# Kernel tuning notes

Measured on AMD Instinct MI355X. Metric: run time of the kernel, lower is better.

Reference implementation:

```python
import jax, jax.numpy as jnp
import numpy as np

B, T, C, H = 2, 2048, 1024, 16
DH = C // H
EPS = 1e-5


def _rotary(t_len, d_head):
    inv_freq = 1.0 / (10000.0 ** (jnp.arange(0, d_head, 2, dtype=jnp.float32) / d_head))
    t = jnp.arange(t_len, dtype=jnp.float32)
    freqs = t[:, None] * inv_freq[None, :]           # [T, dh/2]
    emb = jnp.concatenate([freqs, freqs], axis=-1)    # [T, dh]
    return jnp.cos(emb), jnp.sin(emb)


def _apply_rope(x, cos, sin):
    # x: [B,H,T,dh]; cos/sin: [T,dh]
    d = x.shape[-1]
    x1, x2 = x[..., : d // 2], x[..., d // 2 :]
    x_rot = jnp.concatenate([-x2, x1], axis=-1)
    return x * cos + x_rot * sin


def _decay_mask(t_len, n_head):
    gammas = 1.0 - 2.0 ** (-5.0 - jnp.arange(n_head, dtype=jnp.float32))  # [H]
    n = jnp.arange(t_len)[:, None]
    m = jnp.arange(t_len)[None, :]
    dist = n - m
    decay = gammas[:, None, None] ** jnp.maximum(dist, 0).astype(jnp.float32)
    return jnp.where(dist[None] >= 0, decay, 0.0)  # [H,T,T]


def setup_inputs() -> dict:
    key = jax.random.key(0)
    ks = jax.random.split(key, 7)
    s = 1.0 / np.sqrt(C)
    return {
        "x": jax.random.normal(ks[0], (B, T, C), dtype=jnp.float32),
        "Wq": jax.random.normal(ks[1], (C, C), dtype=jnp.float32) * s,
        "Wk": jax.random.normal(ks[2], (C, C), dtype=jnp.float32) * s,
        "Wv": jax.random.normal(ks[3], (C, C), dtype=jnp.float32) * s,
        "Wo": jax.random.normal(ks[4], (C, C), dtype=jnp.float32) * s,
        "gn_weight": jnp.ones((C,), dtype=jnp.float32),
        "gn_bias": jnp.zeros((C,), dtype=jnp.float32),
    }


def reference(x, Wq, Wk, Wv, Wo, gn_weight, gn_bias):
    b, t, c = x.shape
    # projections (torch Linear: y = x @ W.T), split heads -> [B,H,T,dh]
    def proj(W):
        return jnp.einsum("btc,oc->bto", x, W).reshape(b, t, H, DH).transpose(0, 2, 1, 3)
    q, k, v = proj(Wq), proj(Wk), proj(Wv)

    cos, sin = _rotary(t, DH)
    q = _apply_rope(q, cos, sin)
    k = _apply_rope(k, cos, sin)

    decay = _decay_mask(t, H)                          # [H,T,T]
    qk = jnp.einsum("bhtd,bhsd->bhts", q, k) * (1.0 / np.sqrt(DH))
    qk = qk * decay[None]
    out = jnp.einsum("bhts,bhsd->bhtd", qk, v)         # [B,H,T,dh]

    # GroupNorm with n_head groups over channels, per token
    out = out.transpose(0, 2, 1, 3)                    # [B,T,H,dh]
    mu = jnp.mean(out, axis=-1, keepdims=True)
    var = jnp.mean((out - mu) ** 2, axis=-1, keepdims=True)
    out = (out - mu) * jax.lax.rsqrt(var + EPS)
    out = out * gn_weight.reshape(H, DH) + gn_bias.reshape(H, DH)

    out = out.reshape(b, t, c)
    return jnp.einsum("btc,oc->bto", out, Wo)
```

## Files before the change

### kernel.cpp

```cpp
#include <hip/hip_runtime.h>
#include <stdint.h>

#define B_ 2
#define T_ 2048
#define C_ 1024
#define H_ 16
#define DH_ 64
#define M_ (B_*T_)

typedef short bhalf8 __attribute__((ext_vector_type(8)));
typedef float floatx4 __attribute__((ext_vector_type(4)));

__device__ __forceinline__ short f2bf(float f) {
  unsigned u = __float_as_uint(f);
  u += 0x7fffu + ((u >> 16) & 1u);
  return (short)(u >> 16);
}
__device__ __forceinline__ float bf2f(short s) {
  return __uint_as_float(((unsigned)(unsigned short)s) << 16);
}

__device__ __forceinline__ void gll16(void* lds_dst, const void* g_src) {
  __builtin_amdgcn_global_load_lds(
      reinterpret_cast<const uint32_t __attribute__((address_space(1)))*>(
          reinterpret_cast<uintptr_t>(g_src)),
      reinterpret_cast<uint32_t __attribute__((address_space(3)))*>(
          reinterpret_cast<uintptr_t>(lds_dst)),
      16, 0, 0);
}

__global__ void cvt_all(
    const float* __restrict__ x,  const float* __restrict__ wq,
    const float* __restrict__ wk, const float* __restrict__ wv,
    const float* __restrict__ wo,
    short* __restrict__ xb, short* __restrict__ wqb, short* __restrict__ wkb,
    short* __restrict__ wvb, short* __restrict__ wob)
{
  int i = blockIdx.x * blockDim.x + threadIdx.x;
  const float* s; short* d; int off;
  if (i < (M_*C_/4)) { s = x; d = xb; off = i; }
  else {
    int j = i - M_*C_/4;
    int w = j >> 18;
    off = j & ((1<<18) - 1);
    s = (w==0) ? wq : (w==1) ? wk : (w==2) ? wv : wo;
    d = (w==0) ? wqb : (w==1) ? wkb : (w==2) ? wvb : wob;
  }
  float4 v = ((const float4*)s)[off];
  short4 o;
  o.x = f2bf(v.x); o.y = f2bf(v.y); o.z = f2bf(v.z); o.w = f2bf(v.w);
  ((short4*)d)[off] = o;
}

__global__ __launch_bounds__(512, 2) void gemm_qkv(
    const short* __restrict__ X,
    const short* __restrict__ Wq, const short* __restrict__ Wk, const short* __restrict__ Wv,
    short* __restrict__ Qb, short* __restrict__ Kb, short* __restrict__ Vt)
{
  __shared__ __align__(16) short As[2][256*64];
  __shared__ __align__(16) short Bs[2][256*64];
  const int tid  = threadIdx.x;
  const int lane = tid & 63;
  const int wid  = tid >> 6;
  const int l15  = lane & 15;
  const int quad = lane >> 4;
  const int wr   = wid >> 2;
  const int wc   = wid & 3;
  const int K    = C_;

  const int bid = blockIdx.x;
  const int wg  = (bid & 7) * 24 + (bid >> 3);
  const int nx  = wg % 12;
  const int m0  = (wg / 12) << 8;

  int kind, nloc;
  const short *Ab, *Bb;
  if (nx < 4)      { kind = 0; nloc = nx << 8;       Ab = X  + (size_t)m0*K;   Bb = Wq + (size_t)nloc*K; }
  else if (nx < 8) { kind = 1; nloc = (nx - 4) << 8; Ab = X  + (size_t)m0*K;   Bb = Wk + (size_t)nloc*K; }
  else             { kind = 2; nloc = (nx - 8) << 8; Ab = Wv + (size_t)nloc*K; Bb = X  + (size_t)m0*K;   }

  const int r_loc = tid >> 3;
  const int g_lin = tid & 7;

  auto stageU = [&](short* lds, const short* g, int q, int k0) {
    int row = (q << 6) + r_loc;
    int gs  = g_lin ^ (row & 7);
    gll16(lds + (q << 12) + (wid << 9), g + (size_t)row * K + k0 + (gs << 3));
  };

  floatx4 acc[8][4] = {};

  stageU(&Bs[0][0], Bb, 0, 0); stageU(&Bs[0][0], Bb, 1, 0);
  stageU(&Bs[0][0], Bb, 2, 0); stageU(&Bs[0][0], Bb, 3, 0);
  stageU(&As[0][0], Ab, 0, 0); stageU(&As[0][0], Ab, 2, 0);
  stageU(&As[0][0], Ab, 1, 0); stageU(&As[0][0], Ab, 3, 0);
  asm volatile("s_waitcnt vmcnt(2)" ::: "memory");
  __builtin_amdgcn_s_barrier();
  __builtin_amdgcn_sched_barrier(0);

  for (int t = 0; t < 16; ++t) {
    const int buf = t & 1, nbuf = buf ^ 1;
    const int kn = (t + 1) << 6;
    const bool pf = (t < 15);
    bhalf8 aF[4], bF[4];

#pragma unroll
    for (int i = 0; i < 4; ++i) {
      int row = (wr << 7) + (i << 4) + l15;
      aF[i] = *(const bhalf8*)&As[buf][(row << 6) + ((quad ^ (row & 7)) << 3)];
    }
#pragma unroll
    for (int n = 0; n < 4; ++n) {
      int row = (wc << 6) + (n << 4) + l15;
      bF[n] = *(const bhalf8*)&Bs[buf][(row << 6) + ((quad ^ (row & 7)) << 3)];
    }
    if (pf) { stageU(&Bs[nbuf][0], Bb, 0, kn); stageU(&Bs[nbuf][0], Bb, 1, kn); }
    __builtin_amdgcn_s_barrier();
    asm volatile("s_waitcnt lgkmcnt(0)" ::: "memory");
    __builtin_amdgcn_sched_barrier(0);
    __builtin_amdgcn_s_setprio(1);
#pragma unroll
    for (int i = 0; i < 4; ++i)
#pragma unroll
      for (int n = 0; n < 4; ++n)
        acc[i][n] = __builtin_amdgcn_mfma_f32_16x16x32_bf16(aF[i], bF[n], acc[i][n], 0, 0, 0);
    __builtin_amdgcn_s_setprio(0);
    asm volatile("s_waitcnt vmcnt(2)" ::: "memory");
    __builtin_amdgcn_s_barrier();
    __builtin_amdgcn_sched_barrier(0);

#pragma unroll
    for (int i = 0; i < 4; ++i) {
      int row = (wr << 7) + ((4 + i) << 4) + l15;
      aF[i] = *(const bhalf8*)&As[buf][(row << 6) + ((quad ^ (row & 7)) << 3)];
    }
    if (pf) { stageU(&Bs[nbuf][0], Bb, 2, kn); stageU(&Bs[nbuf][0], Bb, 3, kn); }
    __builtin_amdgcn_s_barrier();
    asm volatile("s_waitcnt lgkmcnt(0)" ::: "memory");
    __builtin_amdgcn_sched_barrier(0);
    __builtin_amdgcn_s_setprio(1);
#pragma unroll
    for (int i = 0; i < 4; ++i)
#pragma unroll
      for (int n = 0; n < 4; ++n)
        acc[4 + i][n] = __builtin_amdgcn_mfma_f32_16x16x32_bf16(aF[i], bF[n], acc[4 + i][n], 0, 0, 0);
    __builtin_amdgcn_s_setprio(0);
    asm volatile("s_waitcnt vmcnt(4)" ::: "memory");
    __builtin_amdgcn_s_barrier();
    __builtin_amdgcn_sched_barrier(0);

#pragma unroll
    for (int i = 0; i < 4; ++i) {
      int row = (wr << 7) + (i << 4) + l15;
      aF[i] = *(const bhalf8*)&As[buf][(row << 6) + (((4 + quad) ^ (row & 7)) << 3)];
    }
#pragma unroll
    for (int n = 0; n < 4; ++n) {
      int row = (wc << 6) + (n << 4) + l15;
      bF[n] = *(const bhalf8*)&Bs[buf][(row << 6) + (((4 + quad) ^ (row & 7)) << 3)];
    }
    if (pf) { stageU(&As[nbuf][0], Ab, 0, kn); stageU(&As[nbuf][0], Ab, 2, kn); }
    __builtin_amdgcn_s_barrier();
    asm volatile("s_waitcnt lgkmcnt(0)" ::: "memory");
    __builtin_amdgcn_sched_barrier(0);
    __builtin_amdgcn_s_setprio(1);
#pragma unroll
    for (int i = 0; i < 4; ++i)
#pragma unroll
      for (int n = 0; n < 4; ++n)
        acc[i][n] = __builtin_amdgcn_mfma_f32_16x16x32_bf16(aF[i], bF[n], acc[i][n], 0, 0, 0);
    __builtin_amdgcn_s_setprio(0);
    asm volatile("s_waitcnt vmcnt(6)" ::: "memory");
    __builtin_amdgcn_s_barrier();
    __builtin_amdgcn_sched_barrier(0);

#pragma unroll
    for (int i = 0; i < 4; ++i) {
      int row = (wr << 7) + ((4 + i) << 4) + l15;
      aF[i] = *(const bhalf8*)&As[buf][(row << 6) + (((4 + quad) ^ (row & 7)) << 3)];
    }
    if (pf) { stageU(&As[nbuf][0], Ab, 1, kn); stageU(&As[nbuf][0], Ab, 3, kn); }
    __builtin_amdgcn_s_barrier();
    asm volatile("s_waitcnt lgkmcnt(0)" ::: "memory");
    __builtin_amdgcn_sched_barrier(0);
    __builtin_amdgcn_s_setprio(1);
#pragma unroll
    for (int i = 0; i < 4; ++i)
#pragma unroll
      for (int n = 0; n < 4; ++n)
        acc[4 + i][n] = __builtin_amdgcn_mfma_f32_16x16x32_bf16(aF[i], bF[n], acc[4 + i][n], 0, 0, 0);
    __builtin_amdgcn_s_setprio(0);
    asm volatile("s_waitcnt vmcnt(2)" ::: "memory");
    __builtin_amdgcn_s_barrier();
    __builtin_amdgcn_sched_barrier(0);
  }

  if (kind < 2) {
    short* Cb = kind ? Kb : Qb;
    const int hh = (nloc + (wc << 6)) >> 6;
    const float frq0 = exp2f((float)l15        * (-0.4152410118609203f));
    const float frq1 = exp2f((float)(l15 + 16) * (-0.4152410118609203f));
#pragma unroll
    for (int m = 0; m < 8; ++m)
#pragma unroll
      for (int r = 0; r < 4; ++r) {
        int n  = m0 + (wr << 7) + (m << 4) + (quad << 2) + r;
        int bb = n >> 11, tt = n & (T_ - 1);
        size_t base = ((size_t)(bb * H_ + hh) * T_ + tt) * DH_;
        float tf = (float)tt;
        {
          float ang = tf * frq0;
          float sn = __sinf(ang), cs = __cosf(ang);
          float xlo = acc[m][0][r], xhi = acc[m][2][r];
          Cb[base + l15]      = f2bf(xlo * cs - xhi * sn);
          Cb[base + l15 + 32] = f2bf(xhi * cs + xlo * sn);
        }
        {
          float ang = tf * frq1;
          float sn = __sinf(ang), cs = __cosf(ang);
          float xlo = acc[m][1][r], xhi = acc[m][3][r];
          Cb[base + l15 + 16] = f2bf(xlo * cs - xhi * sn);
          Cb[base + l15 + 48] = f2bf(xhi * cs + xlo * sn);
        }
      }
  } else {
#pragma unroll
    for (int m = 0; m < 8; ++m)
#pragma unroll
      for (int r = 0; r < 4; ++r) {
        int o = nloc + (wr << 7) + (m << 4) + (quad << 2) + r;
#pragma unroll
        for (int n = 0; n < 4; ++n) {
          int tk = m0 + (wc << 6) + (n << 4) + l15;
          int bb = tk >> 11, tt = tk & (T_ - 1);
          Vt[(size_t)bb * (C_ * T_) + (size_t)o * T_ + tt] = f2bf(acc[m][n][r]);
        }
      }
  }
}

__global__ __launch_bounds__(256) void gemm_out(
    const short* __restrict__ A, const short* __restrict__ Bm, float* __restrict__ Cf)
{
  __shared__ __align__(16) short As[2][128*32];
  __shared__ __align__(16) short Bs[2][64*32];
  const int tid = threadIdx.x, lane = tid & 63, wv = tid >> 6;
  const int l15 = lane & 15, quad = lane >> 4;
  const int n0 = blockIdx.x << 6;
  const int m0 = blockIdx.y << 7;

  const short* Ab = A  + (size_t)m0 * C_;
  const short* Bb = Bm + (size_t)n0 * C_;

  auto stage = [&](int buf, int k0) {
#pragma unroll
    for (int i = 0; i < 2; ++i) {
      int p = (i<<8) + tid, r = p >> 2, go = (p & 3) ^ ((r >> 1) & 3);
      gll16(&As[buf][((i<<8) + (wv<<6))*8], Ab + (size_t)r*C_ + k0 + (go<<3));
    }
    {
      int p = tid, r = p >> 2, go = (p & 3) ^ ((r >> 1) & 3);
      gll16(&Bs[buf][(wv<<6)*8], Bb + (size_t)r*C_ + k0 + (go<<3));
    }
  };

  floatx4 acc[2][4] = {};
  stage(0, 0);
  int cur = 0;
  for (int it = 0; it < 32; ++it) {
    __syncthreads();
    if (it < 31) stage(cur ^ 1, (it + 1) << 5);
    bhalf8 af[2], bfr[4];
#pragma unroll
    for (int rt = 0; rt < 2; ++rt) {
      int row = (wv<<5) + rt*16 + l15;
      af[rt] = *(const bhalf8*)&As[cur][(row<<5) + ((quad ^ ((row>>1)&3))<<3)];
    }
#pragma unroll
    for (int ct = 0; ct < 4; ++ct) {
      int row = ct*16 + l15;
      bfr[ct] = *(const bhalf8*)&Bs[cur][(row<<5) + ((quad ^ ((row>>1)&3))<<3)];
    }
#pragma unroll
    for (int rt = 0; rt < 2; ++rt)
#pragma unroll
      for (int ct = 0; ct < 4; ++ct)
        acc[rt][ct] = __builtin_amdgcn_mfma_f32_16x16x32_bf16(af[rt], bfr[ct], acc[rt][ct], 0, 0, 0);
    cur ^= 1;
  }

#pragma unroll
  for (int rt = 0; rt < 2; ++rt)
#pragma unroll
    for (int r = 0; r < 4; ++r) {
      int n = m0 + (wv<<5) + rt*16 + quad*4 + r;
#pragma unroll
      for (int ct = 0; ct < 4; ++ct)
        Cf[(size_t)n * C_ + n0 + ct*16 + l15] = acc[rt][ct][r];
    }
}

__global__ __launch_bounds__(256) void transpose_k(
    const short* __restrict__ Kb, short* __restrict__ Kt)
{
  __shared__ short tile[64*66];
  const int idx = blockIdx.x, bh = idx >> 5, tc = idx & 31;
  const int t0 = tc << 6;
  const short* src = Kb + ((size_t)bh*T_ + t0) * DH_;
  int row = threadIdx.x >> 2, c0 = (threadIdx.x & 3) << 4;
  *(int4*)&tile[row*66 + c0]     = *(const int4*)&src[row*64 + c0];
  *(int4*)&tile[row*66 + c0 + 8] = *(const int4*)&src[row*64 + c0 + 8];
  __syncthreads();
  short* dst = Kt + (size_t)bh*DH_*T_;
  int d = threadIdx.x >> 2, k0 = (threadIdx.x & 3) << 4;
  short tmp[16];
#pragma unroll
  for (int i = 0; i < 16; ++i) tmp[i] = tile[(k0 + i)*66 + d];
  *(int4*)&dst[(size_t)d*T_ + t0 + k0]     = *(const int4*)&tmp[0];
  *(int4*)&dst[(size_t)d*T_ + t0 + k0 + 8] = *(const int4*)&tmp[8];
}

__global__ __launch_bounds__(256) void seg_state(
    const short* __restrict__ Kt, const short* __restrict__ Vt,
    short* __restrict__ Pseg)
{
  __shared__ __align__(16) short Ks[2][64*64];
  __shared__ __align__(16) short Vs[2][64*64];
  const int tid = threadIdx.x, lane = tid & 63, wv = tid >> 6;
  const int l15 = lane & 15, quad = lane >> 4;
  const int wrow = wv << 4;
  const int bh = blockIdx.x >> 3, p = blockIdx.x & 7;
  const int h = bh & 15;
  const float log2g = log2f(1.f - exp2f(-5.f - (float)h));
  const float g64 = exp2f(log2g * 64.f);

  float wgt[16];
#pragma unroll
  for (int ks = 0; ks < 2; ++ks)
#pragma unroll
    for (int i = 0; i < 8; ++i)
      wgt[ks*8 + i] = exp2f(log2g * (float)(64 - (ks*32 + (quad<<3) + i)));

  const short* Ktg = Kt + (size_t)bh*DH_*T_;
  const short* Vtg = Vt + (size_t)bh*DH_*T_;

  auto stage = [&](int buf, int jc) {
    const int m0 = ((p<<2) + jc) << 6;
#pragma unroll
    for (int i = 0; i < 2; ++i) {
      int slot = (i<<8) + tid;
      int r = slot >> 3, g = (slot & 7) ^ (r & 7);
      gll16(&Ks[buf][((i<<8) + (wv<<6))*8], Ktg + (size_t)r*T_ + m0 + (g<<3));
      gll16(&Vs[buf][((i<<8) + (wv<<6))*8], Vtg + (size_t)r*T_ + m0 + (g<<3));
    }
  };

  floatx4 acc[4] = {};
  stage(0, 0);
  int cur = 0;
  for (int j = 0; j < 4; ++j) {
    __syncthreads();
    if (j < 3) stage(cur ^ 1, j + 1);
#pragma unroll
    for (int ct = 0; ct < 4; ++ct)
#pragma unroll
      for (int r = 0; r < 4; ++r) acc[ct][r] *= g64;
#pragma unroll
    for (int ks = 0; ks < 2; ++ks) {
      int row = wrow + l15;
      bhalf8 va = *(const bhalf8*)&Vs[cur][(row<<6) + ((((ks<<2)+quad) ^ (row&7))<<3)];
      bhalf8 aw;
#pragma unroll
      for (int i = 0; i < 8; ++i) aw[i] = f2bf(bf2f(va[i]) * wgt[ks*8 + i]);
      bhalf8 bk[4];
#pragma unroll
      for (int ct = 0; ct < 4; ++ct) {
        int kr = ct*16 + l15;
        bk[ct] = *(const bhalf8*)&Ks[cur][(kr<<6) + ((((ks<<2)+quad) ^ (kr&7))<<3)];
      }
#pragma unroll
      for (int ct = 0; ct < 4; ++ct)
        acc[ct] = __builtin_amdgcn_mfma_f32_16x16x32_bf16(aw, bk[ct], acc[ct], 0, 0, 0);
    }
    cur ^= 1;
  }
  size_t base = (size_t)(bh*8 + p) * 2 * 4096;
#pragma unroll
  for (int ct = 0; ct < 4; ++ct)
#pragma unroll
    for (int r = 0; r < 4; ++r) {
      int e = wrow + (quad<<2) + r, d = ct*16 + l15;
      float x = acc[ct][r];
      short hi = f2bf(x);
      short lo = f2bf(x - bf2f(hi));
      Pseg[base + e*64 + d]        = hi;
      Pseg[base + 4096 + e*64 + d] = lo;
    }
}

__global__ __launch_bounds__(256) void retention_chunk(
    const short* __restrict__ Qb, const short* __restrict__ Kb,
    const short* __restrict__ Kt, const short* __restrict__ Vt,
    const short* __restrict__ Pseg,
    const float* __restrict__ gnw, const float* __restrict__ gnb,
    short* __restrict__ Xn)
{
  __shared__ __align__(16) short Vs[64*64];
  __shared__ __align__(16) short Kts[64*64];
  __shared__ __align__(16) short KSs[64*64];
  __shared__ __align__(16) short Sh[64*64];
  __shared__ __align__(16) short Sl[64*64];

  const int tid = threadIdx.x, lane = tid & 63, wv = tid >> 6;
  const int l15 = lane & 15, quad = lane >> 4;
  const int wrow = wv << 4;

  const int idx = blockIdx.x;
  const int bh = idx & 31;
  const int cc = idx >> 5;
  const int c  = ((cc & 7) << 2) | (cc >> 3);
  const int p = c >> 2, j = c & 3;
  const int b = bh >> 4, h = bh & 15;
  const int n0 = c << 6;

  const float log2g = log2f(1.f - exp2f(-5.f - (float)h));
  const float g64 = exp2f(log2g * 64.f);

  const short* Qg  = Qb + ((size_t)bh*T_ + n0 + wrow) * DH_;
  const short* Kg  = Kb + (size_t)bh*T_*DH_;
  const short* Ktg = Kt + (size_t)bh*DH_*T_;
  const short* Vtg = Vt + (size_t)bh*DH_*T_;

  bhalf8 aq[2];
#pragma unroll
  for (int ks = 0; ks < 2; ++ks)
    aq[ks] = *(const bhalf8*)(Qg + (size_t)l15*DH_ + ks*32 + quad*8);

  float rowf[4], colf0[4];
#pragma unroll
  for (int r = 0; r < 4; ++r)
    rowf[r] = exp2f(log2g * (float)(wrow + (quad<<2) + r)) * 0.125f;
#pragma unroll
  for (int ct = 0; ct < 4; ++ct)
    colf0[ct] = exp2f(-log2g * (float)(ct*16 + l15));

  const bool has_state = (c > 0);

  floatx4 st[4] = {};
  if (j > 0) {
    float wgt[16];
#pragma unroll
    for (int ks = 0; ks < 2; ++ks)
#pragma unroll
      for (int i = 0; i < 8; ++i)
        wgt[ks*8 + i] = exp2f(log2g * (float)(64 - (ks*32 + (quad<<3) + i)));
    for (int jp = 0; jp < j; ++jp) {
      if (log2g * (float)((j - 1 - jp) << 6) < -34.f) continue;
      const int m0 = ((p<<2) + jp) << 6;
      __syncthreads();
#pragma unroll
      for (int i = 0; i < 2; ++i) {
        int slot = (i<<8) + tid;
        int r = slot >> 3, g = (slot & 7) ^ (r & 7);
        gll16(&Kts[((i<<8) + (wv<<6))*8], Ktg + (size_t)r*T_ + m0 + (g<<3));
        gll16(&Vs[((i<<8) + (wv<<6))*8],  Vtg + (size_t)r*T_ + m0 + (g<<3));
      }
      __syncthreads();
#pragma unroll
      for (int ct = 0; ct < 4; ++ct)
#pragma unroll
        for (int r = 0; r < 4; ++r) st[ct][r] *= g64;
#pragma unroll
      for (int ks = 0; ks < 2; ++ks) {
        int row = wrow + l15;
        bhalf8 va = *(const bhalf8*)&Vs[(row<<6) + ((((ks<<2)+quad) ^ (row&7))<<3)];
        bhalf8 aw;
#pragma unroll
        for (int i = 0; i < 8; ++i) aw[i] = f2bf(bf2f(va[i]) * wgt[ks*8 + i]);
        bhalf8 bk[4];
#pragma unroll
        for (int ct = 0; ct < 4; ++ct) {
          int kr = ct*16 + l15;
          bk[ct] = *(const bhalf8*)&Kts[(kr<<6) + ((((ks<<2)+quad) ^ (kr&7))<<3)];
        }
#pragma unroll
        for (int ct = 0; ct < 4; ++ct)
          st[ct] = __builtin_amdgcn_mfma_f32_16x16x32_bf16(aw, bk[ct], st[ct], 0, 0, 0);
      }
    }
  }
  for (int pp = 0; pp < p; ++pp) {
    float wexp = log2g * (float)(n0 - ((pp + 1) << 8));
    if (wexp < -34.f) continue;
    float w = exp2f(wexp);
    const short* Pg = Pseg + (size_t)(bh*8 + pp) * 2 * 4096;
#pragma unroll
    for (int ct = 0; ct < 4; ++ct)
#pragma unroll
      for (int r = 0; r < 4; ++r) {
        int e = wrow + (quad<<2) + r, d = ct*16 + l15;
        st[ct][r] += w * (bf2f(Pg[e*64 + d]) + bf2f(Pg[4096 + e*64 + d]));
      }
  }
  if (has_state) {
#pragma unroll
    for (int ct = 0; ct < 4; ++ct)
#pragma unroll
      for (int r = 0; r < 4; ++r) {
        int e = wrow + (quad<<2) + r, d = ct*16 + l15;
        float x = st[ct][r];
        short hi = f2bf(x);
        short lo = f2bf(x - bf2f(hi));
        int addr = (e<<6) + ((((d>>3) ^ (e&7))<<3)) + (d&7);
        Sh[addr] = hi; Sl[addr] = lo;
      }
  }

  __syncthreads();
#pragma unroll
  for (int i = 0; i < 2; ++i) {
    int slot = (i<<8) + tid;
    int r = slot >> 3, g = (slot & 7) ^ (r & 7);
    gll16(&KSs[((i<<8) + (wv<<6))*8], Kg  + (size_t)(n0 + r)*DH_ + (g<<3));
    gll16(&Vs[((i<<8) + (wv<<6))*8],  Vtg + (size_t)r*T_ + n0 + (g<<3));
  }
  __syncthreads();

  floatx4 sacc[4] = {};
#pragma unroll
  for (int ks = 0; ks < 2; ++ks) {
    bhalf8 bk[4];
#pragma unroll
    for (int ct = 0; ct < 4; ++ct) {
      int row = ct*16 + l15;
      bk[ct] = *(const bhalf8*)&KSs[(row<<6) + ((((ks<<2)+quad) ^ (row&7))<<3)];
    }
#pragma unroll
    for (int ct = 0; ct < 4; ++ct)
      sacc[ct] = __builtin_amdgcn_mfma_f32_16x16x32_bf16(aq[ks], bk[ct], sacc[ct], 0, 0, 0);
  }
  __syncthreads();
#pragma unroll
  for (int ct = 0; ct < 4; ++ct) {
    float cf = colf0[ct];
    int colg = (ct<<1) + (l15>>3);
    int m = ct*16 + l15;
#pragma unroll
    for (int r = 0; r < 4; ++r) {
      int row = wrow + (quad<<2) + r;
      float v = (row >= m) ? sacc[ct][r] * (rowf[r] * cf) : 0.f;
      KSs[(row<<6) + ((colg ^ ((row>>1)&7))<<3) + (l15&7)] = f2bf(v);
    }
  }
  floatx4 oacc[4] = {};
#pragma unroll
  for (int ks = 0; ks < 2; ++ks) {
    int row = wrow + l15;
    bhalf8 as_ = *(const bhalf8*)&KSs[(row<<6) + ((((ks<<2)+quad) ^ ((row>>1)&7))<<3)];
    bhalf8 bv[4];
#pragma unroll
    for (int ct = 0; ct < 4; ++ct) {
      int vrow = ct*16 + l15;
      bv[ct] = *(const bhalf8*)&Vs[(vrow<<6) + ((((ks<<2)+quad) ^ (vrow&7))<<3)];
    }
#pragma unroll
    for (int ct = 0; ct < 4; ++ct)
      oacc[ct] = __builtin_amdgcn_mfma_f32_16x16x32_bf16(as_, bv[ct], oacc[ct], 0, 0, 0);
  }

  if (has_state) {
    floatx4 iacc[4] = {};
#pragma unroll
    for (int ks = 0; ks < 2; ++ks) {
      bhalf8 bhf[4], blf[4];
#pragma unroll
      for (int ct = 0; ct < 4; ++ct) {
        int er = ct*16 + l15;
        int ga = ((((ks<<2)+quad) ^ (er&7))<<3);
        bhf[ct] = *(const bhalf8*)&Sh[(er<<6) + ga];
        blf[ct] = *(const bhalf8*)&Sl[(er<<6) + ga];
      }
#pragma unroll
      for (int ct = 0; ct < 4; ++ct) {
        iacc[ct] = __builtin_amdgcn_mfma_f32_16x16x32_bf16(aq[ks], bhf[ct], iacc[ct], 0, 0, 0);
        iacc[ct] = __builtin_amdgcn_mfma_f32_16x16x32_bf16(aq[ks], blf[ct], iacc[ct], 0, 0, 0);
      }
    }
#pragma unroll
    for (int ct = 0; ct < 4; ++ct)
#pragma unroll
      for (int r = 0; r < 4; ++r)
        oacc[ct][r] += rowf[r] * iacc[ct][r];
  }

#pragma unroll
  for (int r = 0; r < 4; ++r) {
    float s1 = oacc[0][r] + oacc[1][r] + oacc[2][r] + oacc[3][r];
    float s2 = oacc[0][r]*oacc[0][r] + oacc[1][r]*oacc[1][r]
             + oacc[2][r]*oacc[2][r] + oacc[3][r]*oacc[3][r];
#pragma unroll
    for (int off = 1; off < 16; off <<= 1) {
      s1 += __shfl_xor(s1, off);
      s2 += __shfl_xor(s2, off);
    }
    float mean = s1 * (1.f/64.f);
    float var  = s2 * (1.f/64.f) - mean*mean;
    float rstd = rsqrtf(var + 1e-5f);
    int t = n0 + wrow + (quad<<2) + r;
    size_t obase = ((size_t)b*T_ + t)*C_ + h*DH_;
#pragma unroll
    for (int ct = 0; ct < 4; ++ct) {
      int d = ct*16 + l15;
      float y = (oacc[ct][r] - mean)*rstd*gnw[h*DH_ + d] + gnb[h*DH_ + d];
      Xn[obase + d] = f2bf(y);
    }
  }
}

extern "C" void kernel_launch(void* const* d_in, const int* in_sizes, int n_in,
                              void* d_out, int out_size, void* d_ws, size_t ws_size,
                              hipStream_t stream) {
  (void)in_sizes; (void)n_in; (void)out_size; (void)ws_size;
  const float* x   = (const float*)d_in[0];
  const float* Wq  = (const float*)d_in[1];
  const float* Wk  = (const float*)d_in[2];
  const float* Wv  = (const float*)d_in[3];
  const float* Wo  = (const float*)d_in[4];
  const float* gnw = (const float*)d_in[5];
  const float* gnb = (const float*)d_in[6];
  float* out = (float*)d_out;

  char* ws = (char*)d_ws;
  short* Xb   = (short*)(ws);
  short* Ktb  = (short*)(ws);
  short* Wqb  = (short*)(ws + (8u<<20));
  short* Pseg = (short*)(ws + (8u<<20));
  short* Wkb  = (short*)(ws + (10u<<20));
  short* Wvb  = (short*)(ws + (12u<<20));
  short* Wob  = (short*)(ws + (14u<<20));
  short* Qb   = (short*)(ws + (16u<<20));
  short* Kb   = (short*)(ws + (24u<<20));
  short* Vtw  = (short*)(ws + (32u<<20));
  short* Xn   = (short*)(ws + (40u<<20));

  cvt_all<<<(M_*C_/4 + 4*(C_*C_/4)) / 256, 256, 0, stream>>>(
      x, Wq, Wk, Wv, Wo, Xb, Wqb, Wkb, Wvb, Wob);

  gemm_qkv<<<dim3(192), 512, 0, stream>>>(Xb, Wqb, Wkb, Wvb, Qb, Kb, Vtw);
  transpose_k<<<1024, 256, 0, stream>>>(Kb, Ktb);
  seg_state<<<256, 256, 0, stream>>>(Ktb, Vtw, Pseg);
  retention_chunk<<<1024, 256, 0, stream>>>(Qb, Kb, Ktb, Vtw, Pseg, gnw, gnb, Xn);
  gemm_out<<<dim3(16, 32), 256, 0, stream>>>(Xn, Wob, out);
}
```

Before: 170.2 us.

## Fuse K transpose into QKV GEMM epilogue and deepen gemm_out K-tile

The K-projection epilogue in gemm_qkv now also writes the rotated K values into a swizzled LDS tile, reusing the GEMM staging buffers, and stores a transposed Kt copy directly. This removes the separate transpose_k kernel launch and its global read/write pass. Kt moves to its own workspace region so it no longer aliases Xb, which is still read by the QKV GEMM. Separately, gemm_out now stages 64-wide K tiles with an 8-way XOR swizzle, halving the number of loop iterations and barriers at the cost of more LDS per block.

Result: faster. 165.5 us (-2.8%).

```diff
diff --git a/kernel.cpp b/kernel.cpp
--- a/kernel.cpp
+++ b/kernel.cpp
@@ -55,10 +55,14 @@
 __global__ __launch_bounds__(512, 2) void gemm_qkv(
     const short* __restrict__ X,
     const short* __restrict__ Wq, const short* __restrict__ Wk, const short* __restrict__ Wv,
-    short* __restrict__ Qb, short* __restrict__ Kb, short* __restrict__ Vt)
+    short* __restrict__ Qb, short* __restrict__ Kb, short* __restrict__ Vt,
+    short* __restrict__ Kt)
 {
-  __shared__ __align__(16) short As[2][256*64];
-  __shared__ __align__(16) short Bs[2][256*64];
+  __shared__ __align__(16) short SM[4*256*64];
+  short (*As)[256*64] = (short (*)[256*64])(SM);
+  short (*Bs)[256*64] = (short (*)[256*64])(SM + 2*256*64);
+  short* Ct = SM;
+
   const int tid  = threadIdx.x;
   const int lane = tid & 63;
   const int wid  = tid >> 6;
@@ -200,29 +204,59 @@
     const int hh = (nloc + (wc << 6)) >> 6;
     const float frq0 = exp2f((float)l15        * (-0.4152410118609203f));
     const float frq1 = exp2f((float)(l15 + 16) * (-0.4152410118609203f));
+    const int swz = (l15 & 7) << 3;
 #pragma unroll
     for (int m = 0; m < 8; ++m)
 #pragma unroll
       for (int r = 0; r < 4; ++r) {
-        int n  = m0 + (wr << 7) + (m << 4) + (quad << 2) + r;
+        int tl = (wr << 7) + (m << 4) + (quad << 2) + r;
+        int n  = m0 + tl;
         int bb = n >> 11, tt = n & (T_ - 1);
         size_t base = ((size_t)(bb * H_ + hh) * T_ + tt) * DH_;
         float tf = (float)tt;
+        float v0, v1, v2, v3;
         {
           float ang = tf * frq0;
           float sn = __sinf(ang), cs = __cosf(ang);
           float xlo = acc[m][0][r], xhi = acc[m][2][r];
-          Cb[base + l15]      = f2bf(xlo * cs - xhi * sn);
-          Cb[base + l15 + 32] = f2bf(xhi * cs + xlo * sn);
+          v0 = xlo * cs - xhi * sn;
+          v1 = xhi * cs + xlo * sn;
+          Cb[base + l15]      = f2bf(v0);
+          Cb[base + l15 + 32] = f2bf(v1);
         }
         {
           float ang = tf * frq1;
           float sn = __sinf(ang), cs = __cosf(ang);
           float xlo = acc[m][1][r], xhi = acc[m][3][r];
-          Cb[base + l15 + 16] = f2bf(xlo * cs - xhi * sn);
-          Cb[base + l15 + 48] = f2bf(xhi * cs + xlo * sn);
+          v2 = xlo * cs - xhi * sn;
+          v3 = xhi * cs + xlo * sn;
+          Cb[base + l15 + 16] = f2bf(v2);
+          Cb[base + l15 + 48] = f2bf(v3);
         }
-      }
+        if (kind == 1) {
+          int tswz = tl ^ swz;
+          int cb = (wc << 6);
+          Ct[(cb + l15)      * 256 + tswz] = f2bf(v0);
+          Ct[(cb + l15 + 32) * 256 + tswz] = f2bf(v1);
+          Ct[(cb + l15 + 16) * 256 + tswz] = f2bf(v2);
+          Ct[(cb + l15 + 48) * 256 + tswz] = f2bf(v3);
+        }
+      }
+    if (kind == 1) {
+      __syncthreads();
+      const int hb = nloc >> 6;
+#pragma unroll
+      for (int rr = 0; rr < 16; ++rr) {
+        int lin = rr * 512 + tid;
+        int cc_ = lin >> 5;
+        int g   = lin & 31;
+        bhalf8 v = *(const bhalf8*)&Ct[cc_ * 256 + ((g ^ (cc_ & 7)) << 3)];
+        int tg = m0 + (g << 3);
+        int bb = tg >> 11, tt = tg & (T_ - 1);
+        size_t dst = ((size_t)(bb * H_ + hb + (cc_ >> 6)) * DH_ + (cc_ & 63)) * T_ + tt;
+        *(bhalf8*)&Kt[dst] = v;
+      }
+    }
   } else {
 #pragma unroll
     for (int m = 0; m < 8; ++m)
@@ -242,8 +276,8 @@
 __global__ __launch_bounds__(256) void gemm_out(
     const short* __restrict__ A, const short* __restrict__ Bm, float* __restrict__ Cf)
 {
-  __shared__ __align__(16) short As[2][128*32];
-  __shared__ __align__(16) short Bs[2][64*32];
+  __shared__ __align__(16) short As[2][128*64];
+  __shared__ __align__(16) short Bs[2][64*64];
   const int tid = threadIdx.x, lane = tid & 63, wv = tid >> 6;
   const int l15 = lane & 15, quad = lane >> 4;
   const int n0 = blockIdx.x << 6;
@@ -254,38 +288,44 @@
 
   auto stage = [&](int buf, int k0) {
 #pragma unroll
+    for (int i = 0; i < 4; ++i) {
+      int slot = (i<<8) + tid, r = slot >> 3, g = (slot & 7) ^ (r & 7);
+      gll16(&As[buf][((i<<8) + (wv<<6))*8], Ab + (size_t)r*C_ + k0 + (g<<3));
+    }
+#pragma unroll
     for (int i = 0; i < 2; ++i) {
-      int p = (i<<8) + tid, r = p >> 2, go = (p & 3) ^ ((r >> 1) & 3);
-      gll16(&As[buf][((i<<8) + (wv<<6))*8], Ab + (size_t)r*C_ + k0 + (go<<3));
-    }
-    {
-      int p = tid, r = p >> 2, go = (p & 3) ^ ((r >> 1) & 3);
-      gll16(&Bs[buf][(wv<<6)*8], Bb + (size_t)r*C_ + k0 + (go<<3));
+      int slot = (i<<8) + tid, r = slot >> 3, g = (slot & 7) ^ (r & 7);
+      gll16(&Bs[buf][((i<<8) + (wv<<6))*8], Bb + (size_t)r*C_ + k0 + (g<<3));
     }
   };
 
   floatx4 acc[2][4] = {};
   stage(0, 0);
   int cur = 0;
-  for (int it = 0; it < 32; ++it) {
+  for (int it = 0; it < 16; ++it) {
     __syncthreads();
-    if (it < 31) stage(cur ^ 1, (it + 1) << 5);
-    bhalf8 af[2], bfr[4];
-#pragma unroll
-    for (int rt = 0; rt < 2; ++rt) {
-      int row = (wv<<5) + rt*16 + l15;
-      af[rt] = *(const bhalf8*)&As[cur][(row<<5) + ((quad ^ ((row>>1)&3))<<3)];
-    }
-#pragma unroll
-    for (int ct = 0; ct < 4; ++ct) {
-      int row = ct*16 + l15;
-      bfr[ct] = *(const bhalf8*)&Bs[cur][(row<<5) + ((quad ^ ((row>>1)&3))<<3)];
-    }
-#pragma unroll
-    for (int rt = 0; rt < 2; ++rt)
-#pragma unroll
-      for (int ct = 0; ct < 4; ++ct)
-        acc[rt][ct] = __builtin_amdgcn_mfma_f32_16x16x32_bf16(af[rt], bfr[ct], acc[rt][ct], 0, 0, 0);
+    if (it < 15) stage(cur ^ 1, (it + 1) << 6);
+    bhalf8 af[2][2], bfr[2][4];
+#pragma unroll
+    for (int ks = 0; ks < 2; ++ks) {
+#pragma unroll
+      for (int rt = 0; rt < 2; ++rt) {
+        int row = (wv<<5) + rt*16 + l15;
+        af[ks][rt] = *(const bhalf8*)&As[cur][(row<<6) + ((((ks<<2)+quad) ^ (row&7))<<3)];
+      }
+#pragma unroll
+      for (int ct = 0; ct < 4; ++ct) {
+        int row = ct*16 + l15;
+        bfr[ks][ct] = *(const bhalf8*)&Bs[cur][(row<<6) + ((((ks<<2)+quad) ^ (row&7))<<3)];
+      }
+    }
+#pragma unroll
+    for (int ks = 0; ks < 2; ++ks)
+#pragma unroll
+      for (int rt = 0; rt < 2; ++rt)
+#pragma unroll
+        for (int ct = 0; ct < 4; ++ct)
+          acc[rt][ct] = __builtin_amdgcn_mfma_f32_16x16x32_bf16(af[ks][rt], bfr[ks][ct], acc[rt][ct], 0, 0, 0);
     cur ^= 1;
   }
 
@@ -298,26 +338,6 @@
       for (int ct = 0; ct < 4; ++ct)
         Cf[(size_t)n * C_ + n0 + ct*16 + l15] = acc[rt][ct][r];
     }
-}
-
-__global__ __launch_bounds__(256) void transpose_k(
-    const short* __restrict__ Kb, short* __restrict__ Kt)
-{
-  __shared__ short tile[64*66];
-  const int idx = blockIdx.x, bh = idx >> 5, tc = idx & 31;
-  const int t0 = tc << 6;
-  const short* src = Kb + ((size_t)bh*T_ + t0) * DH_;
-  int row = threadIdx.x >> 2, c0 = (threadIdx.x & 3) << 4;
-  *(int4*)&tile[row*66 + c0]     = *(const int4*)&src[row*64 + c0];
-  *(int4*)&tile[row*66 + c0 + 8] = *(const int4*)&src[row*64 + c0 + 8];
-  __syncthreads();
-  short* dst = Kt + (size_t)bh*DH_*T_;
-  int d = threadIdx.x >> 2, k0 = (threadIdx.x & 3) << 4;
-  short tmp[16];
-#pragma unroll
-  for (int i = 0; i < 16; ++i) tmp[i] = tile[(k0 + i)*66 + d];
-  *(int4*)&dst[(size_t)d*T_ + t0 + k0]     = *(const int4*)&tmp[0];
-  *(int4*)&dst[(size_t)d*T_ + t0 + k0 + 8] = *(const int4*)&tmp[8];
 }
 
 __global__ __launch_bounds__(256) void seg_state(
@@ -632,7 +652,6 @@
 
   char* ws = (char*)d_ws;
   short* Xb   = (short*)(ws);
-  short* Ktb  = (short*)(ws);
   short* Wqb  = (short*)(ws + (8u<<20));
   short* Pseg = (short*)(ws + (8u<<20));
   short* Wkb  = (short*)(ws + (10u<<20));
@@ -642,12 +661,12 @@
   short* Kb   = (short*)(ws + (24u<<20));
   short* Vtw  = (short*)(ws + (32u<<20));
   short* Xn   = (short*)(ws + (40u<<20));
+  short* Ktb  = (short*)(ws + (48u<<20));
 
   cvt_all<<<(M_*C_/4 + 4*(C_*C_/4)) / 256, 256, 0, stream>>>(
       x, Wq, Wk, Wv, Wo, Xb, Wqb, Wkb, Wvb, Wob);
 
-  gemm_qkv<<<dim3(192), 512, 0, stream>>>(Xb, Wqb, Wkb, Wvb, Qb, Kb, Vtw);
-  transpose_k<<<1024, 256, 0, stream>>>(Kb, Ktb);
+  gemm_qkv<<<dim3(192), 512, 0, stream>>>(Xb, Wqb, Wkb, Wvb, Qb, Kb, Vtw, Ktb);
   seg_state<<<256, 256, 0, stream>>>(Ktb, Vtw, Pseg);
   retention_chunk<<<1024, 256, 0, stream>>>(Qb, Kb, Ktb, Vtw, Pseg, gnw, gnb, Xn);
   gemm_out<<<dim3(16, 32), 256, 0, stream>>>(Xn, Wob, out);
```
